# Kernel tuning notes

Hardware: AMD Instinct MI355X
Metric: run time of the kernel (lower is better)

Reference implementation:

```python
import jax, jax.numpy as jnp
import numpy as np

B, S, E = 4, 2048, 1024
H = 16
HD = E // H  # head_dim = 64


def setup_inputs() -> dict:
    key = jax.random.key(0)
    ks = jax.random.split(key, 12)
    sc = 0.02
    return {
        "q_encodings": jax.random.normal(ks[0], (B, S, E), jnp.float32),
        "k_encodings": jax.random.normal(ks[1], (B, S, E), jnp.float32),
        "v_encodings": jax.random.normal(ks[2], (B, S, E), jnp.float32),
        # per-head q/k/v linear weights [H, HD, HD] and biases [H, HD]
        "Wq": jax.random.normal(ks[3], (H, HD, HD), jnp.float32) * sc,
        "bq": jax.random.normal(ks[4], (H, HD), jnp.float32) * sc,
        "Wk": jax.random.normal(ks[5], (H, HD, HD), jnp.float32) * sc,
        "bk": jax.random.normal(ks[6], (H, HD), jnp.float32) * sc,
        "Wv": jax.random.normal(ks[7], (H, HD, HD), jnp.float32) * sc,
        "bv": jax.random.normal(ks[8], (H, HD), jnp.float32) * sc,
        # output projection [E, E] + bias [E]
        "Wp": jax.random.normal(ks[9], (E, E), jnp.float32) * sc,
        "bp": jax.random.normal(ks[10], (E,), jnp.float32) * sc,
        "mask": 1,
    }


def reference(q_encodings, k_encodings, v_encodings, Wq, bq, Wk, bk, Wv, bv, Wp, bp, mask):
    b, s, e = q_encodings.shape
    h, hd, _ = Wq.shape
    split = lambda x: x.reshape(b, s, h, hd)  # per-head slices of n_embd
    # batched per-head linear projections (original loops over heads)
    Q = jnp.einsum('bshd,hde->bshe', split(q_encodings), Wq) + bq
    K = jnp.einsum('bshd,hde->bshe', split(k_encodings), Wk) + bk
    V = jnp.einsum('bshd,hde->bshe', split(v_encodings), Wv) + bv
    # scaled dot-product scores [B,H,S,S]; scale uses head_dim (Attention.n_embd)
    scores = jnp.einsum('bqhd,bkhd->bhqk', Q, K) / jnp.sqrt(jnp.float32(hd))
    if mask:  # static Python flag, matches torch `if mask:`
        causal = jnp.tril(jnp.ones((s, s), jnp.float32))
        scores = scores + jnp.where(causal == 0, jnp.float32(-jnp.inf), jnp.float32(0.0))
    attn = jax.nn.softmax(scores, axis=-1)
    ctx = jnp.einsum('bhqk,bkhd->bqhd', attn, V).reshape(b, s, e)
    return ctx @ Wp + bp
```

## Files before the change

kernel.cpp:

```cpp
#include <hip/hip_runtime.h>
#include <hip/hip_bf16.h>
#include <math.h>

typedef __bf16 bf16;
typedef __bf16 bf16x8 __attribute__((ext_vector_type(8)));
typedef float f32x4 __attribute__((ext_vector_type(4)));
typedef unsigned int u32x2 __attribute__((ext_vector_type(2)));

constexpr int B = 4, S = 2048, E = 1024, H = 16, HD = 64;

constexpr float QSCALE = 0.125f * 1.44269504088896340736f;

static __device__ __forceinline__ float exp2_fast(float x) {
#if __has_builtin(__builtin_amdgcn_exp2f)
    return __builtin_amdgcn_exp2f(x);
#else
    float r; asm("v_exp_f32 %0, %1" : "=v"(r) : "v"(x)); return r;
#endif
}

static __device__ __forceinline__ unsigned pk_bf16(float a, float b) {
    union { bf16 h[2]; unsigned u; } r;
    r.h[0] = (bf16)a; r.h[1] = (bf16)b;
    return r.u;
}

__global__ __launch_bounds__(256) void prep_wqkv(
    const float* __restrict__ Wq, const float* __restrict__ Wk,
    const float* __restrict__ Wv, bf16* __restrict__ Wt)
{
    const int h = blockIdx.x, p = blockIdx.y;
    const float* W = (p == 0) ? Wq : (p == 1) ? Wk : Wv;
    const float scale = (p == 0) ? QSCALE : 1.0f;
    __shared__ float t[64][65];
    const int tid = threadIdx.x;
    #pragma unroll
    for (int i = 0; i < 16; ++i) {
        int idx = tid + i * 256;
        int d = idx >> 6, e = idx & 63;
        t[d][e] = W[(size_t)h * 4096 + d * 64 + e];
    }
    __syncthreads();
    bf16* dst = Wt + ((size_t)p * H + h) * 4096;
    #pragma unroll
    for (int i = 0; i < 16; ++i) {
        int idx = tid + i * 256;
        int e = idx >> 6, d = idx & 63;
        dst[e * 64 + d] = (bf16)(t[d][e] * scale);
    }
}

__global__ __launch_bounds__(256) void qkv_proj(
    const float* __restrict__ xq, const float* __restrict__ xk, const float* __restrict__ xv,
    const bf16* __restrict__ Wt,
    const float* __restrict__ bq, const float* __restrict__ bk, const float* __restrict__ bv,
    bf16* __restrict__ Qb, bf16* __restrict__ Kb, bf16* __restrict__ Vt)
{
    const int b = blockIdx.z, h = blockIdx.y, s0 = blockIdx.x * 128;
    const int tid = threadIdx.x;
    const int w = tid >> 6, l = tid & 63;
    const int l16 = l & 15, lg = l >> 4;
    const size_t bh = (size_t)b * H + h;

    __shared__ __align__(16) bf16 xs[128][64];
    __shared__ __align__(16) bf16 Wl[64][64];
    __shared__ __align__(16) bf16 ts[10240];

    for (int p = 0; p < 3; ++p) {
        const float* x    = (p == 0) ? xq : (p == 1) ? xk : xv;
        const float* bias = (p == 0) ? bq : (p == 1) ? bk : bv;
        const float  bsc  = (p == 0) ? QSCALE : 1.0f;

        __syncthreads();
        #pragma unroll
        for (int i = 0; i < 4; ++i) {
            int idx = tid + i * 256;
            int r = idx >> 3, g = idx & 7;
            const float* src = &x[((size_t)b * S + s0 + r) * E + h * 64 + g * 8];
            float4 f0 = *(const float4*)src;
            float4 f1 = *(const float4*)(src + 4);
            union { bf16 h8[8]; uint4 u; } pk;
            pk.h8[0] = (bf16)f0.x; pk.h8[1] = (bf16)f0.y;
            pk.h8[2] = (bf16)f0.z; pk.h8[3] = (bf16)f0.w;
            pk.h8[4] = (bf16)f1.x; pk.h8[5] = (bf16)f1.y;
            pk.h8[6] = (bf16)f1.z; pk.h8[7] = (bf16)f1.w;
            *(uint4*)&xs[r][(g ^ (r & 7)) * 8] = pk.u;
        }
        const bf16* wsrc = Wt + ((size_t)p * H + h) * 4096;
        #pragma unroll
        for (int i = 0; i < 2; ++i) {
            int idx = tid + i * 256;
            int e = idx >> 3, g = idx & 7;
            *(uint4*)&Wl[e][(g ^ (e & 7)) * 8] = *(const uint4*)(wsrc + e * 64 + g * 8);
        }
        __syncthreads();

        if (p < 2) {
            float bcol[4];
            #pragma unroll
            for (int ei = 0; ei < 4; ++ei)
                bcol[ei] = bias[h * 64 + ei * 16 + l16] * bsc;
            #pragma unroll
            for (int st = 0; st < 2; ++st) {
                const int srow = w * 32 + st * 16 + l16;
                bf16x8 a0 = *(const bf16x8*)&xs[srow][((lg    ) ^ (srow & 7)) * 8];
                bf16x8 a1 = *(const bf16x8*)&xs[srow][((4 + lg) ^ (srow & 7)) * 8];
                #pragma unroll
                for (int ei = 0; ei < 4; ++ei) {
                    const int erow = ei * 16 + l16;
                    bf16x8 b0 = *(const bf16x8*)&Wl[erow][((lg    ) ^ (erow & 7)) * 8];
                    bf16x8 b1 = *(const bf16x8*)&Wl[erow][((4 + lg) ^ (erow & 7)) * 8];
                    f32x4 acc = {0.f, 0.f, 0.f, 0.f};
                    acc = __builtin_amdgcn_mfma_f32_16x16x32_bf16(a0, b0, acc, 0, 0, 0);
                    acc = __builtin_amdgcn_mfma_f32_16x16x32_bf16(a1, b1, acc, 0, 0, 0);
                    #pragma unroll
                    for (int r = 0; r < 4; ++r)
                        ts[(w * 32 + st * 16 + 4 * lg + r) * 80 + ei * 16 + l16] =
                            (bf16)(acc[r] + bcol[ei]);
                }
            }
            __syncthreads();
            bf16* out = (p == 0) ? Qb : Kb;
            #pragma unroll
            for (int i = 0; i < 4; ++i) {
                int idx = tid + i * 256;
                int r = idx >> 3, g = idx & 7;
                uint4 v = *(const uint4*)&ts[r * 80 + g * 8];
                *(uint4*)(out + (bh * S + s0 + r) * 64 + g * 8) = v;
            }
        } else {
            float brow[4];
            #pragma unroll
            for (int r = 0; r < 4; ++r)
                brow[r] = bias[h * 64 + w * 16 + 4 * lg + r];
            const int erow = w * 16 + l16;
            bf16x8 a0 = *(const bf16x8*)&Wl[erow][((lg    ) ^ (erow & 7)) * 8];
            bf16x8 a1 = *(const bf16x8*)&Wl[erow][((4 + lg) ^ (erow & 7)) * 8];
            #pragma unroll
            for (int st = 0; st < 8; ++st) {
                const int srow = st * 16 + l16;
                bf16x8 b0 = *(const bf16x8*)&xs[srow][((lg    ) ^ (srow & 7)) * 8];
                bf16x8 b1 = *(const bf16x8*)&xs[srow][((4 + lg) ^ (srow & 7)) * 8];
                f32x4 acc = {0.f, 0.f, 0.f, 0.f};
                acc = __builtin_amdgcn_mfma_f32_16x16x32_bf16(a0, b0, acc, 0, 0, 0);
                acc = __builtin_amdgcn_mfma_f32_16x16x32_bf16(a1, b1, acc, 0, 0, 0);
                #pragma unroll
                for (int r = 0; r < 4; ++r)
                    ts[(w * 16 + 4 * lg + r) * 136 + st * 16 + l16] =
                        (bf16)(acc[r] + brow[r]);
            }
            __syncthreads();
            #pragma unroll
            for (int i = 0; i < 4; ++i) {
                int idx = tid + i * 256;
                int r = idx >> 4, g = idx & 15;
                uint4 v = *(const uint4*)&ts[r * 136 + g * 8];
                *(uint4*)(Vt + (bh * 64 + r) * S + s0 + g * 8) = v;
            }
        }
    }
}

__global__ __launch_bounds__(256) void prep_wp(const float* __restrict__ Wp,
                                               bf16* __restrict__ Wpt)
{
    __shared__ float t[64][65];
    const int tid = threadIdx.x;
    const int k0 = blockIdx.y * 64, n0 = blockIdx.x * 64;
    #pragma unroll
    for (int i = 0; i < 16; ++i) {
        int idx = tid + i * 256;
        int r = idx >> 6, c = idx & 63;
        t[r][c] = Wp[(size_t)(k0 + r) * E + n0 + c];
    }
    __syncthreads();
    #pragma unroll
    for (int i = 0; i < 16; ++i) {
        int idx = tid + i * 256;
        int r = idx >> 6, c = idx & 63;
        Wpt[(size_t)(n0 + r) * E + k0 + c] = (bf16)t[c][r];
    }
}

__global__ __launch_bounds__(512) void attn(
    const bf16* __restrict__ Qb, const bf16* __restrict__ Kb,
    const bf16* __restrict__ Vt, bf16* __restrict__ ctx)
{
    const int pair = blockIdx.x;
    const int bh   = blockIdx.y;
    const int b = bh >> 4, h = bh & 15;
    const int tid = threadIdx.x;
    const int w = tid >> 6;
    const int l = tid & 63;
    const int l16 = l & 15, lg = l >> 4;

    __shared__ __align__(16) bf16 Kl[2][64][64];
    __shared__ __align__(16) bf16 Vl[2][64][64];
    __shared__ __align__(16) bf16 Pl[8][16][72];

    const bf16* Qp = Qb + (size_t)bh * S * 64;
    const bf16* Kp = Kb + (size_t)bh * S * 64;
    const bf16* Vp = Vt + (size_t)bh * 64 * S;

    const int str = tid >> 3;
    const int stc = tid & 7;
    const int sws = (stc ^ (str & 7)) * 8;

    #pragma unroll 1
    for (int half = 0; half < 2; ++half) {
        const int qt   = half ? (15 - pair) : pair;
        const int qw0  = qt * 128 + w * 16;
        const int qabs = qw0 + l16;
        const int nt   = 2 * qt + 2;

        bf16x8 qf0 = *(const bf16x8*)(Qp + (size_t)qabs * 64 + lg * 8);
        bf16x8 qf1 = *(const bf16x8*)(Qp + (size_t)qabs * 64 + 32 + lg * 8);

        f32x4 o[4] = {};
        float m_run = -1e30f, l_run = 0.f;

        {
            uint4 kreg = *(const uint4*)(Kp + (size_t)str * 64 + stc * 8);
            uint4 vreg = *(const uint4*)(Vp + (size_t)str * S + stc * 8);
            *(uint4*)&Kl[0][str][sws] = kreg;
            *(uint4*)&Vl[0][str][sws] = vreg;
        }
        int cur = 0;
        for (int t = 0; t < nt; ++t) {
            __syncthreads();
            const bool pfv = (t + 1 < nt);
            uint4 kreg, vreg;
            if (pfv) {
                const int kv1 = (t + 1) * 64;
                kreg = *(const uint4*)(Kp + (size_t)(kv1 + str) * 64 + stc * 8);
                vreg = *(const uint4*)(Vp + (size_t)str * S + kv1 + stc * 8);
            }
            const int kv0 = t * 64;
            if (kv0 < qw0 + 16) {
                float p[16];
                #pragma unroll
                for (int s = 0; s < 4; ++s) {
                    f32x4 sc = {0.f, 0.f, 0.f, 0.f};
                    const int row = 16 * s + l16;
                    bf16x8 ka = *(const bf16x8*)&Kl[cur][row][(lg       ^ (l16 & 7)) * 8];
                    bf16x8 kb = *(const bf16x8*)&Kl[cur][row][((4 + lg) ^ (l16 & 7)) * 8];
                    sc = __builtin_amdgcn_mfma_f32_16x16x32_bf16(ka, qf0, sc, 0, 0, 0);
                    sc = __builtin_amdgcn_mfma_f32_16x16x32_bf16(kb, qf1, sc, 0, 0, 0);
                    p[4 * s + 0] = sc[0]; p[4 * s + 1] = sc[1];
                    p[4 * s + 2] = sc[2]; p[4 * s + 3] = sc[3];
                }

                if (kv0 + 63 > qw0) {
                    #pragma unroll
                    for (int i = 0; i < 16; ++i) {
                        const int kvloc = 16 * (i >> 2) + 4 * lg + (i & 3);
                        if (kv0 + kvloc > qabs) p[i] = -1e30f;
                    }
                }

                float mx = p[0];
                #pragma unroll
                for (int i = 1; i < 16; ++i) mx = fmaxf(mx, p[i]);
                mx = fmaxf(mx, __shfl_xor(mx, 16));
                mx = fmaxf(mx, __shfl_xor(mx, 32));
                const float m_new = fmaxf(m_run, mx);
                const float corr = exp2_fast(m_run - m_new);
                float sum = 0.f;
                #pragma unroll
                for (int i = 0; i < 16; ++i) { p[i] = exp2_fast(p[i] - m_new); sum += p[i]; }
                sum += __shfl_xor(sum, 16);
                sum += __shfl_xor(sum, 32);
                l_run = l_run * corr + sum;
                m_run = m_new;
                #pragma unroll
                for (int ds = 0; ds < 4; ++ds) {
                    o[ds][0] *= corr; o[ds][1] *= corr;
                    o[ds][2] *= corr; o[ds][3] *= corr;
                }

                #pragma unroll
                for (int s = 0; s < 4; ++s) {
                    u32x2 pw;
                    pw[0] = pk_bf16(p[4 * s + 0], p[4 * s + 1]);
                    pw[1] = pk_bf16(p[4 * s + 2], p[4 * s + 3]);
                    *(u32x2*)&Pl[w][l16][16 * s + 4 * lg] = pw;
                }
                asm volatile("s_waitcnt lgkmcnt(0)" ::: "memory");
                bf16x8 pf0 = *(const bf16x8*)&Pl[w][l16][8 * lg];
                bf16x8 pf1 = *(const bf16x8*)&Pl[w][l16][32 + 8 * lg];

                #pragma unroll
                for (int ds = 0; ds < 4; ++ds) {
                    const int row = 16 * ds + l16;
                    bf16x8 v0 = *(const bf16x8*)&Vl[cur][row][(lg       ^ (l16 & 7)) * 8];
                    bf16x8 v1 = *(const bf16x8*)&Vl[cur][row][((4 + lg) ^ (l16 & 7)) * 8];
                    o[ds] = __builtin_amdgcn_mfma_f32_16x16x32_bf16(v0, pf0, o[ds], 0, 0, 0);
                    o[ds] = __builtin_amdgcn_mfma_f32_16x16x32_bf16(v1, pf1, o[ds], 0, 0, 0);
                }
            }
            if (pfv) {
                *(uint4*)&Kl[cur ^ 1][str][sws] = kreg;
                *(uint4*)&Vl[cur ^ 1][str][sws] = vreg;
            }
            cur ^= 1;
        }

        const float il = 1.0f / l_run;
        bf16* crow = ctx + ((size_t)b * S + qabs) * E + h * 64;
        #pragma unroll
        for (int ds = 0; ds < 4; ++ds) {
            u32x2 pw;
            pw[0] = pk_bf16(o[ds][0] * il, o[ds][1] * il);
            pw[1] = pk_bf16(o[ds][2] * il, o[ds][3] * il);
            *(u32x2*)(crow + 16 * ds + 4 * lg) = pw;
        }
    }
}

__global__ __launch_bounds__(256) void out_gemm(
    const bf16* __restrict__ A, const bf16* __restrict__ Bt,
    const float* __restrict__ bp, float* __restrict__ C)
{
    const int n0 = blockIdx.x * 128, m0 = blockIdx.y * 128;
    const int tid = threadIdx.x;
    const int w = tid >> 6, l = tid & 63;
    const int l16 = l & 15, lg = l >> 4;
    const int wm = w >> 1, wn = w & 1;

    __shared__ __align__(16) bf16 Al[128][64];
    __shared__ __align__(16) bf16 Bl[128][64];

    f32x4 acc[4][4] = {};

    for (int k0 = 0; k0 < E; k0 += 64) {
        __syncthreads();
        #pragma unroll
        for (int i = 0; i < 4; ++i) {
            int row = (tid >> 3) + i * 32;
            int c = tid & 7;
            int cs = c ^ (row & 7);
            *(uint4*)&Al[row][cs * 8] =
                *(const uint4*)(A + (size_t)(m0 + row) * E + k0 + c * 8);
            *(uint4*)&Bl[row][cs * 8] =
                *(const uint4*)(Bt + (size_t)(n0 + row) * E + k0 + c * 8);
        }
        __syncthreads();

        #pragma unroll
        for (int ks = 0; ks < 2; ++ks) {
            bf16x8 af[4], bfr[4];
            #pragma unroll
            for (int mi = 0; mi < 4; ++mi) {
                int r = wm * 64 + mi * 16 + l16;
                af[mi] = *(const bf16x8*)&Al[r][((ks * 4 + lg) ^ (r & 7)) * 8];
            }
            #pragma unroll
            for (int ni = 0; ni < 4; ++ni) {
                int r = wn * 64 + ni * 16 + l16;
                bfr[ni] = *(const bf16x8*)&Bl[r][((ks * 4 + lg) ^ (r & 7)) * 8];
            }
            #pragma unroll
            for (int mi = 0; mi < 4; ++mi)
                #pragma unroll
                for (int ni = 0; ni < 4; ++ni)
                    acc[mi][ni] = __builtin_amdgcn_mfma_f32_16x16x32_bf16(
                        af[mi], bfr[ni], acc[mi][ni], 0, 0, 0);
        }
    }

    #pragma unroll
    for (int ni = 0; ni < 4; ++ni) {
        const int col = n0 + wn * 64 + ni * 16 + l16;
        const float bias = bp[col];
        #pragma unroll
        for (int mi = 0; mi < 4; ++mi) {
            #pragma unroll
            for (int e = 0; e < 4; ++e) {
                int row = m0 + wm * 64 + mi * 16 + 4 * lg + e;
                C[(size_t)row * E + col] = acc[mi][ni][e] + bias;
            }
        }
    }
}

extern "C" void kernel_launch(void* const* d_in, const int* in_sizes, int n_in,
                              void* d_out, int out_size, void* d_ws, size_t ws_size,
                              hipStream_t stream)
{
    const float* xq = (const float*)d_in[0];
    const float* xk = (const float*)d_in[1];
    const float* xv = (const float*)d_in[2];
    const float* Wq = (const float*)d_in[3];
    const float* bq = (const float*)d_in[4];
    const float* Wk = (const float*)d_in[5];
    const float* bk = (const float*)d_in[6];
    const float* Wv = (const float*)d_in[7];
    const float* bv = (const float*)d_in[8];
    const float* Wp = (const float*)d_in[9];
    const float* bp = (const float*)d_in[10];
    float* out = (float*)d_out;

    char* ws = (char*)d_ws;
    const size_t sz_bhse = (size_t)B * H * S * HD;
    bf16* Qb  = (bf16*)ws;  ws += sz_bhse * 2;
    bf16* Kb  = (bf16*)ws;  ws += sz_bhse * 2;
    bf16* Vtw = (bf16*)ws;  ws += sz_bhse * 2;
    bf16* ctx = (bf16*)ws;  ws += (size_t)B * S * E * 2;
    bf16* Wpt = (bf16*)ws;  ws += (size_t)E * E * 2;
    bf16* Wt3 = (bf16*)ws;  ws += (size_t)3 * H * HD * HD * 2;

    prep_wqkv<<<dim3(H, 3), 256, 0, stream>>>(Wq, Wk, Wv, Wt3);
    qkv_proj<<<dim3(S / 128, H, B), 256, 0, stream>>>(xq, xk, xv, Wt3,
                                                      bq, bk, bv, Qb, Kb, Vtw);
    prep_wp<<<dim3(E / 64, E / 64), 256, 0, stream>>>(Wp, Wpt);
    attn<<<dim3(8, B * H), 512, 0, stream>>>(Qb, Kb, Vtw, ctx);
    out_gemm<<<dim3(E / 128, (B * S) / 128), 256, 0, stream>>>(ctx, Wpt, bp, out);
}
```

Before: 132.2 us.

## Skip online-softmax rescale under threshold, add MFMA priority and precomputed LDS offsets

Result: faster. 128.4 us (-2.9%).

```diff
diff --git a/kernel.cpp b/kernel.cpp
--- a/kernel.cpp
+++ b/kernel.cpp
@@ -10,6 +10,7 @@
 constexpr int B = 4, S = 2048, E = 1024, H = 16, HD = 64;
 
 constexpr float QSCALE = 0.125f * 1.44269504088896340736f;
+constexpr float DTHR = 11.5f;
 
 static __device__ __forceinline__ float exp2_fast(float x) {
 #if __has_builtin(__builtin_amdgcn_exp2f)
@@ -206,6 +207,16 @@
     const int stc = tid & 7;
     const int sws = (stc ^ (str & 7)) * 8;
 
+    int foff0[4], foff1[4];
+    #pragma unroll
+    for (int s = 0; s < 4; ++s) {
+        foff0[s] = (16 * s + l16) * 64 + ((lg    ) ^ (l16 & 7)) * 8;
+        foff1[s] = (16 * s + l16) * 64 + ((4 + lg) ^ (l16 & 7)) * 8;
+    }
+    bf16* Plw = &Pl[w][0][0];
+    const int pwr = l16 * 72 + 4 * lg;
+    const int prd = l16 * 72 + 8 * lg;
+
     #pragma unroll 1
     for (int half = 0; half < 2; ++half) {
         const int qt   = half ? (15 - pair) : pair;
@@ -237,18 +248,22 @@
             }
             const int kv0 = t * 64;
             if (kv0 < qw0 + 16) {
+                const bf16* Kbase = &Kl[cur][0][0];
+                const bf16* Vbase = &Vl[cur][0][0];
+
                 float p[16];
+                __builtin_amdgcn_s_setprio(1);
                 #pragma unroll
                 for (int s = 0; s < 4; ++s) {
                     f32x4 sc = {0.f, 0.f, 0.f, 0.f};
-                    const int row = 16 * s + l16;
-                    bf16x8 ka = *(const bf16x8*)&Kl[cur][row][(lg       ^ (l16 & 7)) * 8];
-                    bf16x8 kb = *(const bf16x8*)&Kl[cur][row][((4 + lg) ^ (l16 & 7)) * 8];
+                    bf16x8 ka = *(const bf16x8*)(Kbase + foff0[s]);
+                    bf16x8 kb = *(const bf16x8*)(Kbase + foff1[s]);
                     sc = __builtin_amdgcn_mfma_f32_16x16x32_bf16(ka, qf0, sc, 0, 0, 0);
                     sc = __builtin_amdgcn_mfma_f32_16x16x32_bf16(kb, qf1, sc, 0, 0, 0);
                     p[4 * s + 0] = sc[0]; p[4 * s + 1] = sc[1];
                     p[4 * s + 2] = sc[2]; p[4 * s + 3] = sc[3];
                 }
+                __builtin_amdgcn_s_setprio(0);
 
                 if (kv0 + 63 > qw0) {
                     #pragma unroll
@@ -263,40 +278,44 @@
                 for (int i = 1; i < 16; ++i) mx = fmaxf(mx, p[i]);
                 mx = fmaxf(mx, __shfl_xor(mx, 16));
                 mx = fmaxf(mx, __shfl_xor(mx, 32));
-                const float m_new = fmaxf(m_run, mx);
-                const float corr = exp2_fast(m_run - m_new);
+                if (!__all(mx <= m_run + DTHR)) {
+                    const float m_new = fmaxf(m_run, mx);
+                    const float corr = exp2_fast(m_run - m_new);
+                    l_run *= corr;
+                    #pragma unroll
+                    for (int ds = 0; ds < 4; ++ds) {
+                        o[ds][0] *= corr; o[ds][1] *= corr;
+                        o[ds][2] *= corr; o[ds][3] *= corr;
+                    }
+                    m_run = m_new;
+                }
                 float sum = 0.f;
                 #pragma unroll
-                for (int i = 0; i < 16; ++i) { p[i] = exp2_fast(p[i] - m_new); sum += p[i]; }
+                for (int i = 0; i < 16; ++i) { p[i] = exp2_fast(p[i] - m_run); sum += p[i]; }
                 sum += __shfl_xor(sum, 16);
                 sum += __shfl_xor(sum, 32);
-                l_run = l_run * corr + sum;
-                m_run = m_new;
-                #pragma unroll
-                for (int ds = 0; ds < 4; ++ds) {
-                    o[ds][0] *= corr; o[ds][1] *= corr;
-                    o[ds][2] *= corr; o[ds][3] *= corr;
-                }
+                l_run += sum;
 
                 #pragma unroll
                 for (int s = 0; s < 4; ++s) {
                     u32x2 pw;
                     pw[0] = pk_bf16(p[4 * s + 0], p[4 * s + 1]);
                     pw[1] = pk_bf16(p[4 * s + 2], p[4 * s + 3]);
-                    *(u32x2*)&Pl[w][l16][16 * s + 4 * lg] = pw;
+                    *(u32x2*)(Plw + pwr + 16 * s) = pw;
                 }
                 asm volatile("s_waitcnt lgkmcnt(0)" ::: "memory");
-                bf16x8 pf0 = *(const bf16x8*)&Pl[w][l16][8 * lg];
-                bf16x8 pf1 = *(const bf16x8*)&Pl[w][l16][32 + 8 * lg];
-
+                bf16x8 pf0 = *(const bf16x8*)(Plw + prd);
+                bf16x8 pf1 = *(const bf16x8*)(Plw + prd + 32);
+
+                __builtin_amdgcn_s_setprio(1);
                 #pragma unroll
                 for (int ds = 0; ds < 4; ++ds) {
-                    const int row = 16 * ds + l16;
-                    bf16x8 v0 = *(const bf16x8*)&Vl[cur][row][(lg       ^ (l16 & 7)) * 8];
-                    bf16x8 v1 = *(const bf16x8*)&Vl[cur][row][((4 + lg) ^ (l16 & 7)) * 8];
+                    bf16x8 v0 = *(const bf16x8*)(Vbase + foff0[ds]);
+                    bf16x8 v1 = *(const bf16x8*)(Vbase + foff1[ds]);
                     o[ds] = __builtin_amdgcn_mfma_f32_16x16x32_bf16(v0, pf0, o[ds], 0, 0, 0);
                     o[ds] = __builtin_amdgcn_mfma_f32_16x16x32_bf16(v1, pf1, o[ds], 0, 0, 0);
                 }
+                __builtin_amdgcn_s_setprio(0);
             }
             if (pfv) {
                 *(uint4*)&Kl[cur ^ 1][str][sws] = kreg;
```
